# Optimization experiments

Hardware: AMD Instinct MI355X
Metric: run time of the kernel (lower is better)

Reference implementation:

```python
import jax, jax.numpy as jnp
import numpy as np

S = 4096
T_STEPS = 2048

def setup_inputs() -> dict:
    key = jax.random.key(0)
    k1, k2, k3 = jax.random.split(key, 3)
    # initial log-prior over S states
    log_M0 = jax.nn.log_softmax(jax.random.normal(k1, (S,), dtype=jnp.float32))
    # transition log-probs: log_trans[i, j] = log p(x_t = i | x_{t-1} = j)
    # (logsumexp in the torch code is over dim=1 = previous state, so columns normalize)
    log_trans = jax.nn.log_softmax(jax.random.normal(k2, (S, S), dtype=jnp.float32), axis=0)
    # per-step emission log-likelihoods log f_t(y_t | x_t), t = 0..T
    log_emit = 0.5 * jax.random.normal(k3, (T_STEPS + 1, S), dtype=jnp.float32)
    return {"log_M0": log_M0, "log_trans": log_trans, "log_emit": log_emit, "T": T_STEPS}

def reference(log_M0, log_trans, log_emit, T):
    # initialise(): unnormalized filter at t=0
    unnorm0 = log_M0 + log_emit[0]                       # [S]
    lf0 = jax.nn.logsumexp(unnorm0)                      # scalar log-normalizer
    filt0 = unnorm0 - lf0

    def step(carry, emit_t):
        filt, lik = carry
        # prediction_i = logsumexp_j( filter_j + log_trans[i, j] )
        pred = jax.nn.logsumexp(filt[None, :] + log_trans, axis=1)   # [S]
        unnorm = pred + emit_t                                        # [S]
        lf = jax.nn.logsumexp(unnorm)
        return (unnorm - lf, lik + lf), None

    (_, likelihood), _ = jax.lax.scan(step, (filt0, lf0), log_emit[1:T + 1])
    # forward() returns the accumulated sum of per-step likelihood factors = total log-likelihood
    return likelihood
```

## Files before the change

kernel.cpp:

```cpp
#include <hip/hip_runtime.h>

#define SS 4096
#define TT 2048

typedef float v4f __attribute__((ext_vector_type(4)));
typedef float v2f __attribute__((ext_vector_type(2)));
typedef unsigned u2 __attribute__((ext_vector_type(2)));


__device__ __forceinline__ void llc_load2(const v4f* p, v4f& a, v4f& b) {
  asm volatile(
      "global_load_dwordx4 %0, %2, off sc0 sc1\n\t"
      "global_load_dwordx4 %1, %3, off sc0 sc1\n\t"
      "s_waitcnt vmcnt(0)"
      : "=&v"(a), "=&v"(b)
      : "v"(p), "v"(p + 512)
      : "memory");
}

__device__ __forceinline__ void llc_load4x4(const v4f* p,
                                            v4f& a, v4f& b, v4f& c, v4f& d) {
  asm volatile(
      "global_load_dwordx4 %0, %4, off sc0 sc1\n\t"
      "global_load_dwordx4 %1, %5, off sc0 sc1\n\t"
      "global_load_dwordx4 %2, %6, off sc0 sc1\n\t"
      "global_load_dwordx4 %3, %7, off sc0 sc1\n\t"
      "s_waitcnt vmcnt(0)"
      : "=&v"(a), "=&v"(b), "=&v"(c), "=&v"(d)
      : "v"(p), "v"(p + 256), "v"(p + 512), "v"(p + 768)
      : "memory");
}

__device__ __forceinline__ void llc_sent4(const float* p0, const float* p1,
                                          const float* p2, const float* p3,
                                          float& a, float& b, float& c, float& d) {
  asm volatile(
      "global_load_dword %0, %4, off sc0 sc1\n\t"
      "global_load_dword %1, %5, off sc0 sc1\n\t"
      "global_load_dword %2, %6, off sc0 sc1\n\t"
      "global_load_dword %3, %7, off sc0 sc1\n\t"
      "s_waitcnt vmcnt(0)"
      : "=&v"(a), "=&v"(b), "=&v"(c), "=&v"(d)
      : "v"(p0), "v"(p1), "v"(p2), "v"(p3)
      : "memory");
}

__device__ __forceinline__ void llc_store2_drain(float* p, v2f v) {
  asm volatile("global_store_dwordx2 %0, %1, off sc0 sc1\n\t"
               "s_waitcnt vmcnt(0)"
               :: "v"(p), "v"(v) : "memory");
}

__device__ __forceinline__ void straggle_tick(int lane) {
  float dummy;
  asm volatile("ds_read_b32 %0, %1\n\t"
               "s_waitcnt lgkmcnt(0)"
               : "=v"(dummy) : "v"(lane << 7) : "memory");
  asm volatile("" :: "v"(dummy));
}


__device__ __forceinline__ unsigned short f2bf_rn(float f) {
  unsigned int u = __float_as_uint(f);
  u += 0x7FFFu + ((u >> 16) & 1u);
  return (unsigned short)(u >> 16);
}

__device__ __forceinline__ unsigned pkbf(float a, float b) {
  return (unsigned)f2bf_rn(a) | ((unsigned)f2bf_rn(b) << 16);
}

__device__ __forceinline__ float blo(unsigned w) { return __uint_as_float(w << 16); }
__device__ __forceinline__ float bhi(unsigned w) { return __uint_as_float(w & 0xFFFF0000u); }

__device__ __forceinline__ v4f fma4(u2 e, v4f q, v4f a) {
  a.x = fmaf(blo(e.x), q.x, a.x);
  a.y = fmaf(bhi(e.x), q.y, a.y);
  a.z = fmaf(blo(e.y), q.z, a.z);
  a.w = fmaf(bhi(e.y), q.w, a.w);
  return a;
}

__device__ __forceinline__ unsigned orsgn(v4f v, unsigned e) {
  return (__float_as_uint(v.x) ^ e) | (__float_as_uint(v.y) ^ e)
       | (__float_as_uint(v.z) ^ e) | (__float_as_uint(v.w) ^ e);
}

__global__ void init_q(const float* __restrict__ m0, const float* __restrict__ emit,
                       float* __restrict__ q) {
  int i = blockIdx.x * 256 + threadIdx.x;
  q[i] = __expf(m0[i] + emit[i]);
}

#define K16(X) X(0) X(1) X(2) X(3) X(4) X(5) X(6) X(7) \
               X(8) X(9) X(10) X(11) X(12) X(13) X(14) X(15)

__global__ void __launch_bounds__(512, 1) __attribute__((amdgpu_waves_per_eu(2, 2)))
hmm_fwd(const float* __restrict__ lt, const float* __restrict__ emit,
        float* q, float* out) {
  __shared__ float qs[2][SS];
  __shared__ float wsum[4];
  const int b    = blockIdx.x;
  const int tid  = threadIdx.x;
  const int wave = tid >> 6;
  const int lane = tid & 63;
  const int row0 = (b << 4) + (wave << 1);

#define DECL_E(k) u2 e0_##k, e1_##k;
  K16(DECL_E)
#undef DECL_E

  {
    const float* s0 = lt + (size_t)row0 * SS + (lane << 2);
    const float* s1 = s0 + SS;
#define INIT_E(k) { \
    v4f t0 = *(const v4f*)(s0 + ((k) << 8)); \
    v4f t1 = *(const v4f*)(s1 + ((k) << 8)); \
    e0_##k = (u2){pkbf(__expf(t0.x), __expf(t0.y)), pkbf(__expf(t0.z), __expf(t0.w))}; \
    e1_##k = (u2){pkbf(__expf(t1.x), __expf(t1.y)), pkbf(__expf(t1.z), __expf(t1.w))}; }
    K16(INIT_E)
#undef INIT_E
  }

  for (int t = 1; t <= TT; ++t) {
    v2f em;
    if (lane == 0) em = *(const v2f*)(emit + (size_t)t * SS + row0);

    const unsigned e = (unsigned)(((t - 1) >> 1) & 1) << 31;
    {
      const v4f* qsrc4 = (const v4f*)(q + ((t - 1) & 1) * SS);
      v4f va, vb;
      llc_load2(qsrc4 + tid, va, vb);
      unsigned o = orsgn(va, e) | orsgn(vb, e);
      if (o >> 31) {
        const float* qw = (const float*)qsrc4;
        const float* p0 = qw + (tid << 2);
        const float* p1 = p0 + 2;
        const float* p2 = p0 + 2048;
        const float* p3 = p0 + 2050;
        for (;;) {
          straggle_tick(lane);
          float s0v, s1v, s2v, s3v;
          llc_sent4(p0, p1, p2, p3, s0v, s1v, s2v, s3v);
          unsigned so = (__float_as_uint(s0v) ^ e) | (__float_as_uint(s1v) ^ e)
                      | (__float_as_uint(s2v) ^ e) | (__float_as_uint(s3v) ^ e);
          if (!(so >> 31)) break;
        }
        llc_load2(qsrc4 + tid, va, vb);
      }
      v4f* qsb = (v4f*)qs[t & 1];
      qsb[tid]       = va;
      qsb[tid + 512] = vb;
    }
    __syncthreads();

    v4f a0 = {0.f, 0.f, 0.f, 0.f}, a1 = a0;
    const v4f* qv4 = (const v4f*)qs[t & 1];
#define FMA_K(k) { \
    v4f qv = qv4[((k) << 6) + lane]; \
    a0 = fma4(e0_##k, qv, a0);  a1 = fma4(e1_##k, qv, a1); }
    K16(FMA_K)
#undef FMA_K

    float acc0 = (a0.x + a0.y) + (a0.z + a0.w);
    float acc1 = (a1.x + a1.y) + (a1.z + a1.w);
#pragma unroll
    for (int m = 32; m > 0; m >>= 1) {
      acc0 += __shfl_xor(acc0, m);
      acc1 += __shfl_xor(acc1, m);
    }

    if (lane == 0) {
      float scale = ((t & 255) == 0) ? 0x1p-46f : 1.0f;
      if (!(t & 1)) scale = -scale;
      v2f r;
      r.x = acc0 * (__expf(em.x) * scale);
      r.y = acc1 * (__expf(em.y) * scale);
      llc_store2_drain(q + (t & 1) * SS + row0, r);
    }
  }

  if (b == 0) {
    float s = 0.f;
    if (tid < 256) {
      const v4f* qf4 = (const v4f*)q;
      v4f va, vb, vc, vd;
      for (;;) {
        llc_load4x4(qf4 + tid, va, vb, vc, vd);
        unsigned o = orsgn(va, 0) | orsgn(vb, 0) | orsgn(vc, 0) | orsgn(vd, 0);
        if (!(o >> 31)) break;
      }
      s = va.x + va.y + va.z + va.w + vb.x + vb.y + vb.z + vb.w
        + vc.x + vc.y + vc.z + vc.w + vd.x + vd.y + vd.z + vd.w;
#pragma unroll
      for (int m = 32; m > 0; m >>= 1) s += __shfl_xor(s, m);
      if (lane == 0) wsum[wave] = s;
    }
    __syncthreads();
    if (tid == 0) {
      float tot = wsum[0] + wsum[1] + wsum[2] + wsum[3];
      out[0] = logf(tot) + 368.0f * 0.693147180559945f;
    }
  }
}

extern "C" void kernel_launch(void* const* d_in, const int* in_sizes, int n_in,
                              void* d_out, int out_size, void* d_ws, size_t ws_size,
                              hipStream_t stream) {
  const float* log_M0    = (const float*)d_in[0];
  const float* log_trans = (const float*)d_in[1];
  const float* log_emit  = (const float*)d_in[2];

  float* q   = (float*)d_ws;
  float* out = (float*)d_out;

  hipLaunchKernelGGL(init_q, dim3(SS / 256), dim3(256), 0, stream, log_M0, log_emit, q);
  hipLaunchKernelGGL(hmm_fwd, dim3(256), dim3(512), 0, stream, log_trans, log_emit, q, out);
}
```

Baseline: 4.722 ms.

## Fuse init into forward kernel and prefetch next-step emissions

Removes the separate init_q launch by having each block compute and store its own initial q rows at the start of the persistent kernel. The loop is unrolled by two with ping-pong registers, so the emission row for step t+1 is loaded asynchronously right after the barrier and its latency is hidden behind the FMA and reduction work. The exp of the emission is computed by all lanes before the shuffle reduction instead of only by lane 0 after it. The init stores rely on the first step's sign-flag polling to see all rows written by other blocks before they are consumed.

```diff
diff --git a/kernel.cpp b/kernel.cpp
--- a/kernel.cpp
+++ b/kernel.cpp
@@ -86,18 +86,12 @@
        | (__float_as_uint(v.z) ^ e) | (__float_as_uint(v.w) ^ e);
 }
 
-__global__ void init_q(const float* __restrict__ m0, const float* __restrict__ emit,
-                       float* __restrict__ q) {
-  int i = blockIdx.x * 256 + threadIdx.x;
-  q[i] = __expf(m0[i] + emit[i]);
-}
-
 #define K16(X) X(0) X(1) X(2) X(3) X(4) X(5) X(6) X(7) \
                X(8) X(9) X(10) X(11) X(12) X(13) X(14) X(15)
 
 __global__ void __launch_bounds__(512, 1) __attribute__((amdgpu_waves_per_eu(2, 2)))
-hmm_fwd(const float* __restrict__ lt, const float* __restrict__ emit,
-        float* q, float* out) {
+hmm_fwd(const float* __restrict__ lt, const float* __restrict__ m0,
+        const float* __restrict__ emit, float* q, float* out) {
   __shared__ float qs[2][SS];
   __shared__ float wsum[4];
   const int b    = blockIdx.x;
@@ -105,6 +99,19 @@
   const int wave = tid >> 6;
   const int lane = tid & 63;
   const int row0 = (b << 4) + (wave << 1);
+
+  {
+    v2f m0v = *(const v2f*)(m0 + row0);
+    v2f e0v = *(const v2f*)(emit + row0);
+    v2f q0;
+    q0.x = __expf(m0v.x + e0v.x);
+    q0.y = __expf(m0v.y + e0v.y);
+    if (lane == 0) llc_store2_drain(q + row0, q0);
+  }
+
+  v2f emA, emB;
+  asm volatile("global_load_dwordx2 %0, %1, off"
+               : "=&v"(emA) : "v"(emit + (size_t)SS + row0) : "memory");
 
 #define DECL_E(k) u2 e0_##k, e1_##k;
   K16(DECL_E)
@@ -122,66 +129,72 @@
 #undef INIT_E
   }
 
-  for (int t = 1; t <= TT; ++t) {
-    v2f em;
-    if (lane == 0) em = *(const v2f*)(emit + (size_t)t * SS + row0);
-
-    const unsigned e = (unsigned)(((t - 1) >> 1) & 1) << 31;
-    {
-      const v4f* qsrc4 = (const v4f*)(q + ((t - 1) & 1) * SS);
-      v4f va, vb;
-      llc_load2(qsrc4 + tid, va, vb);
-      unsigned o = orsgn(va, e) | orsgn(vb, e);
-      if (o >> 31) {
-        const float* qw = (const float*)qsrc4;
-        const float* p0 = qw + (tid << 2);
-        const float* p1 = p0 + 2;
-        const float* p2 = p0 + 2048;
-        const float* p3 = p0 + 2050;
-        for (;;) {
-          straggle_tick(lane);
-          float s0v, s1v, s2v, s3v;
-          llc_sent4(p0, p1, p2, p3, s0v, s1v, s2v, s3v);
-          unsigned so = (__float_as_uint(s0v) ^ e) | (__float_as_uint(s1v) ^ e)
-                      | (__float_as_uint(s2v) ^ e) | (__float_as_uint(s3v) ^ e);
-          if (!(so >> 31)) break;
-        }
-        llc_load2(qsrc4 + tid, va, vb);
-      }
-      v4f* qsb = (v4f*)qs[t & 1];
-      qsb[tid]       = va;
-      qsb[tid + 512] = vb;
-    }
-    __syncthreads();
-
-    v4f a0 = {0.f, 0.f, 0.f, 0.f}, a1 = a0;
-    const v4f* qv4 = (const v4f*)qs[t & 1];
 #define FMA_K(k) { \
     v4f qv = qv4[((k) << 6) + lane]; \
     a0 = fma4(e0_##k, qv, a0);  a1 = fma4(e1_##k, qv, a1); }
-    K16(FMA_K)
+
+#define STEP(T, EMC, EMN) { \
+    const unsigned e = (unsigned)(((unsigned)((T) - 1) >> 1) & 1) << 31; \
+    { \
+      const v4f* qsrc4 = (const v4f*)(q + (((T) - 1) & 1) * SS); \
+      v4f va, vb; \
+      llc_load2(qsrc4 + tid, va, vb); \
+      unsigned o = orsgn(va, e) | orsgn(vb, e); \
+      if (o >> 31) { \
+        const float* qw = (const float*)qsrc4; \
+        const float* p0 = qw + (tid << 2); \
+        const float* p1 = p0 + 2; \
+        const float* p2 = p0 + 2048; \
+        const float* p3 = p0 + 2050; \
+        for (;;) { \
+          straggle_tick(lane);    \
+          float s0v, s1v, s2v, s3v; \
+          llc_sent4(p0, p1, p2, p3, s0v, s1v, s2v, s3v); \
+          unsigned so = (__float_as_uint(s0v) ^ e) | (__float_as_uint(s1v) ^ e) \
+                      | (__float_as_uint(s2v) ^ e) | (__float_as_uint(s3v) ^ e); \
+          if (!(so >> 31)) break; \
+        } \
+        llc_load2(qsrc4 + tid, va, vb); \
+      } \
+      v4f* qsb = (v4f*)qs[(T) & 1]; \
+      qsb[tid]       = va; \
+      qsb[tid + 512] = vb; \
+    } \
+    __syncthreads();    \
+    if ((T) < TT) { \
+      asm volatile("global_load_dwordx2 %0, %1, off" \
+                   : "=&v"(EMN) \
+                   : "v"(emit + (size_t)((T) + 1) * SS + row0) : "memory"); \
+    } \
+    v4f a0 = {0.f, 0.f, 0.f, 0.f}, a1 = a0; \
+    const v4f* qv4 = (const v4f*)qs[(T) & 1]; \
+    K16(FMA_K) \
+    float scale = (((T) & 255) == 0) ? 0x1p-46f : 1.0f;   \
+    if (!((T) & 1)) scale = -scale;                        \
+    v2f ex;    \
+    ex.x = __expf(EMC.x) * scale; \
+    ex.y = __expf(EMC.y) * scale; \
+    float acc0 = (a0.x + a0.y) + (a0.z + a0.w); \
+    float acc1 = (a1.x + a1.y) + (a1.z + a1.w); \
+    _Pragma("unroll") \
+    for (int m = 32; m > 0; m >>= 1) { \
+      acc0 += __shfl_xor(acc0, m); \
+      acc1 += __shfl_xor(acc1, m); \
+    } \
+    v2f r; \
+    r.x = acc0 * ex.x; \
+    r.y = acc1 * ex.y; \
+    if (lane == 0) llc_store2_drain(q + ((T) & 1) * SS + row0, r); \
+  }
+
+  for (int t = 1; t <= TT; t += 2) {
+    STEP(t,     emA, emB)
+    STEP(t + 1, emB, emA)
+  }
+#undef STEP
 #undef FMA_K
 
-    float acc0 = (a0.x + a0.y) + (a0.z + a0.w);
-    float acc1 = (a1.x + a1.y) + (a1.z + a1.w);
-#pragma unroll
-    for (int m = 32; m > 0; m >>= 1) {
-      acc0 += __shfl_xor(acc0, m);
-      acc1 += __shfl_xor(acc1, m);
-    }
-
-    if (lane == 0) {
-      float scale = ((t & 255) == 0) ? 0x1p-46f : 1.0f;
-      if (!(t & 1)) scale = -scale;
-      v2f r;
-      r.x = acc0 * (__expf(em.x) * scale);
-      r.y = acc1 * (__expf(em.y) * scale);
-      llc_store2_drain(q + (t & 1) * SS + row0, r);
-    }
-  }
-
   if (b == 0) {
-    float s = 0.f;
     if (tid < 256) {
       const v4f* qf4 = (const v4f*)q;
       v4f va, vb, vc, vd;
@@ -190,8 +203,8 @@
         unsigned o = orsgn(va, 0) | orsgn(vb, 0) | orsgn(vc, 0) | orsgn(vd, 0);
         if (!(o >> 31)) break;
       }
-      s = va.x + va.y + va.z + va.w + vb.x + vb.y + vb.z + vb.w
-        + vc.x + vc.y + vc.z + vc.w + vd.x + vd.y + vd.z + vd.w;
+      float s = va.x + va.y + va.z + va.w + vb.x + vb.y + vb.z + vb.w
+              + vc.x + vc.y + vc.z + vc.w + vd.x + vd.y + vd.z + vd.w;
 #pragma unroll
       for (int m = 32; m > 0; m >>= 1) s += __shfl_xor(s, m);
       if (lane == 0) wsum[wave] = s;
@@ -214,6 +227,6 @@
   float* q   = (float*)d_ws;
   float* out = (float*)d_out;
 
-  hipLaunchKernelGGL(init_q, dim3(SS / 256), dim3(256), 0, stream, log_M0, log_emit, q);
-  hipLaunchKernelGGL(hmm_fwd, dim3(256), dim3(512), 0, stream, log_trans, log_emit, q, out);
-}
+  hipLaunchKernelGGL(hmm_fwd, dim3(256), dim3(512), 0, stream,
+                     log_trans, log_M0, log_emit, q, out);
+}
```

After: 5.513 ms. +16.7%, slower.

## Compute GEMV from each thread's own q slice with reduce-scatter, fuse init

Applied to the files above, without the earlier changes.

Each thread now keeps fp32 exp(transition) values for 16 rows and only the 8 columns it already loads from global q, so the per-step staging of the full q vector into LDS goes away. Partial row sums are combined with a butterfly reduce-scatter across lanes, then a small cross-wave LDS exchange. The bf16 packing is dropped, which removes the unpack ALU work but raises register use. The init_q kernel is folded into the main kernel, saving one launch, but the first step now relies on the workspace's sign state for its synchronisation.

```diff
diff --git a/kernel.cpp b/kernel.cpp
--- a/kernel.cpp
+++ b/kernel.cpp
@@ -5,7 +5,6 @@
 
 typedef float v4f __attribute__((ext_vector_type(4)));
 typedef float v2f __attribute__((ext_vector_type(2)));
-typedef unsigned u2 __attribute__((ext_vector_type(2)));
 
 
 __device__ __forceinline__ void llc_load2(const v4f* p, v4f& a, v4f& b) {
@@ -59,46 +58,18 @@
   asm volatile("" :: "v"(dummy));
 }
 
-
-__device__ __forceinline__ unsigned short f2bf_rn(float f) {
-  unsigned int u = __float_as_uint(f);
-  u += 0x7FFFu + ((u >> 16) & 1u);
-  return (unsigned short)(u >> 16);
-}
-
-__device__ __forceinline__ unsigned pkbf(float a, float b) {
-  return (unsigned)f2bf_rn(a) | ((unsigned)f2bf_rn(b) << 16);
-}
-
-__device__ __forceinline__ float blo(unsigned w) { return __uint_as_float(w << 16); }
-__device__ __forceinline__ float bhi(unsigned w) { return __uint_as_float(w & 0xFFFF0000u); }
-
-__device__ __forceinline__ v4f fma4(u2 e, v4f q, v4f a) {
-  a.x = fmaf(blo(e.x), q.x, a.x);
-  a.y = fmaf(bhi(e.x), q.y, a.y);
-  a.z = fmaf(blo(e.y), q.z, a.z);
-  a.w = fmaf(bhi(e.y), q.w, a.w);
-  return a;
-}
-
 __device__ __forceinline__ unsigned orsgn(v4f v, unsigned e) {
   return (__float_as_uint(v.x) ^ e) | (__float_as_uint(v.y) ^ e)
        | (__float_as_uint(v.z) ^ e) | (__float_as_uint(v.w) ^ e);
 }
 
-__global__ void init_q(const float* __restrict__ m0, const float* __restrict__ emit,
-                       float* __restrict__ q) {
-  int i = blockIdx.x * 256 + threadIdx.x;
-  q[i] = __expf(m0[i] + emit[i]);
-}
-
 #define K16(X) X(0) X(1) X(2) X(3) X(4) X(5) X(6) X(7) \
                X(8) X(9) X(10) X(11) X(12) X(13) X(14) X(15)
 
 __global__ void __launch_bounds__(512, 1) __attribute__((amdgpu_waves_per_eu(2, 2)))
-hmm_fwd(const float* __restrict__ lt, const float* __restrict__ emit,
-        float* q, float* out) {
-  __shared__ float qs[2][SS];
+hmm_fwd(const float* __restrict__ lt, const float* __restrict__ lm0,
+        const float* __restrict__ emit, float* q, float* out) {
+  __shared__ float part[2][8 * 17];
   __shared__ float wsum[4];
   const int b    = blockIdx.x;
   const int tid  = threadIdx.x;
@@ -106,18 +77,25 @@
   const int lane = tid & 63;
   const int row0 = (b << 4) + (wave << 1);
 
-#define DECL_E(k) u2 e0_##k, e1_##k;
+  {
+    v2f m0v = *(const v2f*)(lm0 + row0);
+    v2f e0v = *(const v2f*)(emit + row0);
+    v2f q0;
+    q0.x = __expf(m0v.x + e0v.x);
+    q0.y = __expf(m0v.y + e0v.y);
+    if (lane == 0) llc_store2_drain(q + row0, q0);
+  }
+
+#define DECL_E(r) v4f eA_##r, eB_##r;
   K16(DECL_E)
 #undef DECL_E
-
   {
-    const float* s0 = lt + (size_t)row0 * SS + (lane << 2);
-    const float* s1 = s0 + SS;
-#define INIT_E(k) { \
-    v4f t0 = *(const v4f*)(s0 + ((k) << 8)); \
-    v4f t1 = *(const v4f*)(s1 + ((k) << 8)); \
-    e0_##k = (u2){pkbf(__expf(t0.x), __expf(t0.y)), pkbf(__expf(t0.z), __expf(t0.w))}; \
-    e1_##k = (u2){pkbf(__expf(t1.x), __expf(t1.y)), pkbf(__expf(t1.z), __expf(t1.w))}; }
+    const float* baseE = lt + ((size_t)(b << 4)) * SS + (tid << 2);
+#define INIT_E(r) { \
+    v4f tA = *(const v4f*)(baseE + (size_t)(r) * SS); \
+    v4f tB = *(const v4f*)(baseE + (size_t)(r) * SS + 2048); \
+    eA_##r = (v4f){__expf(tA.x), __expf(tA.y), __expf(tA.z), __expf(tA.w)}; \
+    eB_##r = (v4f){__expf(tB.x), __expf(tB.y), __expf(tB.z), __expf(tB.w)}; }
     K16(INIT_E)
 #undef INIT_E
   }
@@ -127,10 +105,10 @@
     if (lane == 0) em = *(const v2f*)(emit + (size_t)t * SS + row0);
 
     const unsigned e = (unsigned)(((t - 1) >> 1) & 1) << 31;
+    const v4f* qsrc4 = (const v4f*)(q + ((t - 1) & 1) * SS);
+    v4f va, vb;
+    llc_load2(qsrc4 + tid, va, vb);
     {
-      const v4f* qsrc4 = (const v4f*)(q + ((t - 1) & 1) * SS);
-      v4f va, vb;
-      llc_load2(qsrc4 + tid, va, vb);
       unsigned o = orsgn(va, e) | orsgn(vb, e);
       if (o >> 31) {
         const float* qw = (const float*)qsrc4;
@@ -148,40 +126,68 @@
         }
         llc_load2(qsrc4 + tid, va, vb);
       }
-      v4f* qsb = (v4f*)qs[t & 1];
-      qsb[tid]       = va;
-      qsb[tid + 512] = vb;
-    }
+    }
+
+#define DECL_H(r) float h##r;
+    K16(DECL_H)
+#undef DECL_H
+#define GEMV_R(r) { \
+    v4f p = eA_##r * va + eB_##r * vb; \
+    h##r = (p.x + p.y) + (p.z + p.w); }
+    K16(GEMV_R)
+#undef GEMV_R
+
+    const bool b5 = (lane & 32) != 0;
+    const bool b4 = (lane & 16) != 0;
+    const bool b3 = (lane & 8) != 0;
+    const bool b2 = (lane & 4) != 0;
+    float n0, n1, n2, n3, n4, n5, n6, n7;
+#define RS32(i, A, B) { \
+    float kk = b5 ? (B) : (A); \
+    float ss = b5 ? (A) : (B); \
+    n##i = kk + __shfl_xor(ss, 32); }
+    RS32(0, h0, h8)  RS32(1, h1, h9)  RS32(2, h2, h10) RS32(3, h3, h11)
+    RS32(4, h4, h12) RS32(5, h5, h13) RS32(6, h6, h14) RS32(7, h7, h15)
+#undef RS32
+    float mm0, mm1, mm2, mm3;
+#define RS16(i, A, B) { \
+    float kk = b4 ? (B) : (A); \
+    float ss = b4 ? (A) : (B); \
+    mm##i = kk + __shfl_xor(ss, 16); }
+    RS16(0, n0, n4) RS16(1, n1, n5) RS16(2, n2, n6) RS16(3, n3, n7)
+#undef RS16
+    float pp0, pp1;
+#define RS8(i, A, B) { \
+    float kk = b3 ? (B) : (A); \
+    float ss = b3 ? (A) : (B); \
+    pp##i = kk + __shfl_xor(ss, 8); }
+    RS8(0, mm0, mm2) RS8(1, mm1, mm3)
+#undef RS8
+    float s = (b2 ? pp1 : pp0) + __shfl_xor(b2 ? pp0 : pp1, 4);
+    s += __shfl_xor(s, 2);
+    s += __shfl_xor(s, 1);
+
+    if (!(lane & 3)) part[t & 1][wave * 17 + (lane >> 2)] = s;
     __syncthreads();
 
-    v4f a0 = {0.f, 0.f, 0.f, 0.f}, a1 = a0;
-    const v4f* qv4 = (const v4f*)qs[t & 1];
-#define FMA_K(k) { \
-    v4f qv = qv4[((k) << 6) + lane]; \
-    a0 = fma4(e0_##k, qv, a0);  a1 = fma4(e1_##k, qv, a1); }
-    K16(FMA_K)
-#undef FMA_K
-
-    float acc0 = (a0.x + a0.y) + (a0.z + a0.w);
-    float acc1 = (a1.x + a1.y) + (a1.z + a1.w);
-#pragma unroll
-    for (int m = 32; m > 0; m >>= 1) {
-      acc0 += __shfl_xor(acc0, m);
-      acc1 += __shfl_xor(acc1, m);
-    }
+    const float* pb = part[t & 1];
+    float x = pb[(lane & 7) * 17 + (wave << 1) + ((lane >> 3) & 1)];
+    x += __shfl_xor(x, 1);
+    x += __shfl_xor(x, 2);
+    x += __shfl_xor(x, 4);
+    float y = __shfl_xor(x, 8);
 
     if (lane == 0) {
       float scale = ((t & 255) == 0) ? 0x1p-46f : 1.0f;
       if (!(t & 1)) scale = -scale;
       v2f r;
-      r.x = acc0 * (__expf(em.x) * scale);
-      r.y = acc1 * (__expf(em.y) * scale);
+      r.x = x * (__expf(em.x) * scale);
+      r.y = y * (__expf(em.y) * scale);
       llc_store2_drain(q + (t & 1) * SS + row0, r);
     }
   }
 
   if (b == 0) {
-    float s = 0.f;
     if (tid < 256) {
       const v4f* qf4 = (const v4f*)q;
       v4f va, vb, vc, vd;
@@ -190,8 +196,8 @@
         unsigned o = orsgn(va, 0) | orsgn(vb, 0) | orsgn(vc, 0) | orsgn(vd, 0);
         if (!(o >> 31)) break;
       }
-      s = va.x + va.y + va.z + va.w + vb.x + vb.y + vb.z + vb.w
-        + vc.x + vc.y + vc.z + vc.w + vd.x + vd.y + vd.z + vd.w;
+      float s = va.x + va.y + va.z + va.w + vb.x + vb.y + vb.z + vb.w
+              + vc.x + vc.y + vc.z + vc.w + vd.x + vd.y + vd.z + vd.w;
 #pragma unroll
       for (int m = 32; m > 0; m >>= 1) s += __shfl_xor(s, m);
       if (lane == 0) wsum[wave] = s;
@@ -214,6 +220,6 @@
   float* q   = (float*)d_ws;
   float* out = (float*)d_out;
 
-  hipLaunchKernelGGL(init_q, dim3(SS / 256), dim3(256), 0, stream, log_M0, log_emit, q);
-  hipLaunchKernelGGL(hmm_fwd, dim3(256), dim3(512), 0, stream, log_trans, log_emit, q, out);
-}
+  hipLaunchKernelGGL(hmm_fwd, dim3(256), dim3(512), 0, stream,
+                     log_trans, log_M0, log_emit, q, out);
+}
```

New measurement: 4.588 ms. 1.03x faster.
